# Performance work log

Hardware: AMD Instinct MI355X
Metric: run time of the kernel (lower is better)

Reference implementation:

```python
import jax, jax.numpy as jnp
import numpy as np

B, T = 8, 1024
BIG = 1e9

def _lin_init(k, fan_in, fan_out):
    return jax.random.normal(k, (fan_in, fan_out), dtype=jnp.float32) / np.sqrt(fan_in).astype(np.float32)

def setup_inputs() -> dict:
    key = jax.random.key(0)
    ks = jax.random.split(key, 10)
    return {
        "time_step": jax.random.uniform(ks[0], (B, T), dtype=jnp.float32),
        "event": jax.random.randint(ks[1], (B, T), 0, 4),
        "mkt_state": jax.random.randint(ks[2], (B, T), 0, 3),
        "mu_w1": _lin_init(ks[3], 4, 16), "mu_b1": jnp.zeros((16,), jnp.float32),
        "mu_w2": _lin_init(ks[4], 16, 1), "mu_b2": jnp.zeros((1,), jnp.float32),
        "a_w1": _lin_init(ks[5], 11, 16), "a_b1": jnp.zeros((16,), jnp.float32),
        "a_w2": _lin_init(ks[6], 16, 1), "a_b2": jnp.zeros((1,), jnp.float32),
        "d_w1": _lin_init(ks[7], 11, 16), "d_b1": jnp.zeros((16,), jnp.float32),
        "d_w2": _lin_init(ks[8], 16, 1), "d_b2": jnp.zeros((1,), jnp.float32),
    }

def _mlp(x, w1, b1, w2, b2):
    # Linear -> ReLU -> Linear -> Softplus
    return jax.nn.softplus(jax.nn.relu(x @ w1 + b1) @ w2 + b2)

def reference(time_step, event, mkt_state,
              mu_w1, mu_b1, mu_w2, mu_b2,
              a_w1, a_b1, a_w2, a_b2,
              d_w1, d_b1, d_w2, d_b2):
    Bs, Ts = event.shape
    I = Ts - 1  # number of source events
    seq_dt = time_step[:, 1:]                                   # [B, T-1]
    timestep = jnp.concatenate(
        [jnp.zeros((Bs, 1), seq_dt.dtype), jnp.cumsum(seq_dt, axis=-1)], axis=-1)  # [B, T]

    ev = jax.nn.one_hot(event, 4, dtype=jnp.float32)            # [B, T, 4]
    st = jax.nn.one_hot(mkt_state, 3, dtype=jnp.float32)        # [B, T, 3]
    eye4 = jnp.eye(4, dtype=jnp.float32)

    # relation_matrix[b,i,j] = [event_oh(b,i), state_oh(b,i), onehot(j)]  -> [B, I, 4, 11]
    rel = jnp.concatenate([
        jnp.broadcast_to(ev[:, :I, None, :], (Bs, I, 4, 4)),
        jnp.broadcast_to(st[:, :I, None, :], (Bs, I, 4, 3)),
        jnp.broadcast_to(eye4[None, None], (Bs, I, 4, 4)),
    ], axis=-1)

    # dt_matrix[b,i,t] = timestep[b,t] - timestep[b,i], non-positive -> BIG
    dt = timestep[:, None, :] - timestep[:, :I, None]           # [B, I, T]
    dt = jnp.where(dt > 0, dt, BIG)

    # mu: identical MLP applied to eye(4), broadcast to [B, T, 4, 1]
    mu_base = _mlp(eye4, mu_w1, mu_b1, mu_w2, mu_b2)            # [4, 1]
    mu = jnp.broadcast_to(mu_base[None, None], (Bs, Ts, 4, 1))

    alpha = jnp.swapaxes(_mlp(rel, a_w1, a_b1, a_w2, a_b2), 2, 3)  # [B, I, 1, 4]
    delta = jnp.swapaxes(_mlp(rel, d_w1, d_b1, d_w2, d_b2), 2, 3)  # [B, I, 1, 4]

    mask = jnp.triu(jnp.ones((I, I), jnp.float32))              # [I, J]
    dtj = dt[:, :, 1:, None]                                    # [B, I, J, 1]
    # causal exp-decay excitation summed over source events i
    excite = (alpha * jnp.exp(-delta * dtj) * mask[None, :, :, None]).sum(axis=1)  # [B, J, 4]

    intens_matrix = mu[:, 1:, :, 0] + excite                    # [B, T-1, 4]
    return (intens_matrix, mu, alpha, delta)
```

## Files before the change

### kernel.cpp

```cpp
#include <hip/hip_runtime.h>

#define TT 1024
#define BB 8
#define II 1023
#define OFF_INTENS 0
#define OFF_MU     32736
#define OFF_ALPHA  65504
#define OFF_DELTA  98240

__device__ __forceinline__ float softplus_f(float x) {
    return fmaxf(x, 0.f) + log1pf(expf(-fabsf(x)));
}

__global__ __launch_bounds__(256) void k_prep(
    const float* __restrict__ time_step,
    const float* __restrict__ mw1, const float* __restrict__ mb1,
    const float* __restrict__ mw2, const float* __restrict__ mb2,
    const float* __restrict__ aw1, const float* __restrict__ ab1,
    const float* __restrict__ aw2, const float* __restrict__ ab2,
    const float* __restrict__ dw1, const float* __restrict__ db1,
    const float* __restrict__ dw2, const float* __restrict__ db2,
    float* __restrict__ ws)
{
    __shared__ float lds[BB * TT];
    const int tid = threadIdx.x;
    for (int idx = tid; idx < BB * TT; idx += 256) lds[idx] = time_step[idx];
    __syncthreads();

    if (tid < 8) {
        const int b = tid;
        float run = 0.f;
        ws[b * TT] = 0.f;
        for (int t = 1; t < TT; ++t) {
            run += lds[b * TT + t];
            ws[b * TT + t] = run;
        }
    } else if (tid >= 64 && tid < 160) {
        const int idx = tid - 64;
        const int c   = (idx < 48) ? idx : idx - 48;
        const bool isA = idx < 48;
        const float* w1 = isA ? aw1 : dw1;
        const float* b1 = isA ? ab1 : db1;
        const float* w2 = isA ? aw2 : dw2;
        const float* b2 = isA ? ab2 : db2;
        const int e = c / 12, s = (c % 12) >> 2, k = c & 3;
        float acc = 0.f;
        #pragma unroll
        for (int n = 0; n < 16; ++n) {
            float h = w1[e * 16 + n] + w1[(4 + s) * 16 + n] + w1[(7 + k) * 16 + n] + b1[n];
            acc += fmaxf(h, 0.f) * w2[n];
        }
        ws[BB * TT + 2 * c + (isA ? 0 : 1)] = softplus_f(acc + b2[0]);
    } else if (tid >= 160 && tid < 164) {
        const int k = tid - 160;
        float acc = 0.f;
        #pragma unroll
        for (int n = 0; n < 16; ++n)
            acc += fmaxf(mw1[k * 16 + n] + mb1[n], 0.f) * mw2[n];
        ws[BB * TT + 96 + k] = softplus_f(acc + mb2[0]);
    }
}

__global__ __launch_bounds__(256) void k_main(
    const int* __restrict__ event, const int* __restrict__ mkt,
    const float* __restrict__ ws, float* __restrict__ out)
{
    __shared__ float  ts_l[TT];
    __shared__ float2 ad_l[TT * 4];
    const int tid = threadIdx.x;
    const int b   = blockIdx.y;
    const int jt  = blockIdx.x;
    const float2* adtab = (const float2*)(ws + BB * TT);
    const float*  mu_g  = ws + BB * TT + 96;

    for (int t = tid; t < TT; t += 256) ts_l[t] = ws[b * TT + t];
    for (int idx = tid; idx < TT * 4; idx += 256) {
        const int i = idx >> 2, k = idx & 3;
        const int e = event[b * TT + i];
        const int s = mkt[b * TT + i];
        ad_l[idx] = adtab[(e * 3 + s) * 4 + k];
    }
    __syncthreads();

    const int s  = tid & 3;
    const int k  = (tid >> 2) & 3;
    const int jj = tid >> 4;
    const int j  = jt * 16 + jj;

    float acc = 0.f;
    if (j < II) {
        const float tsj1 = ts_l[j + 1];
        #pragma unroll 4
        for (int i = s; i <= j; i += 4) {
            const float2 ad = ad_l[(i << 2) | k];
            float dt = tsj1 - ts_l[i];
            dt = (dt > 0.f) ? dt : 1e9f;
            acc += ad.x * __expf(-ad.y * dt);
        }
    }
    acc += __shfl_xor(acc, 1, 64);
    acc += __shfl_xor(acc, 2, 64);

    const float muk = mu_g[k];
    if (j < II) {
        const int base = (b * II + j) * 4 + k;
        if (s == 0)      out[OFF_INTENS + base] = muk + acc;
        else if (s == 1) out[OFF_ALPHA  + base] = ad_l[(j << 2) | k].x;
        else if (s == 2) out[OFF_DELTA  + base] = ad_l[(j << 2) | k].y;
    }
    if (s == 3) out[OFF_MU + (b * TT + j) * 4 + k] = muk;
}

extern "C" void kernel_launch(void* const* d_in, const int* in_sizes, int n_in,
                              void* d_out, int out_size, void* d_ws, size_t ws_size,
                              hipStream_t stream) {
    const float* time_step = (const float*)d_in[0];
    const int*   event     = (const int*)  d_in[1];
    const int*   mkt       = (const int*)  d_in[2];
    const float* mw1 = (const float*)d_in[3];
    const float* mb1 = (const float*)d_in[4];
    const float* mw2 = (const float*)d_in[5];
    const float* mb2 = (const float*)d_in[6];
    const float* aw1 = (const float*)d_in[7];
    const float* ab1 = (const float*)d_in[8];
    const float* aw2 = (const float*)d_in[9];
    const float* ab2 = (const float*)d_in[10];
    const float* dw1 = (const float*)d_in[11];
    const float* db1 = (const float*)d_in[12];
    const float* dw2 = (const float*)d_in[13];
    const float* db2 = (const float*)d_in[14];
    float* ws  = (float*)d_ws;
    float* out = (float*)d_out;

    k_prep<<<1, 256, 0, stream>>>(time_step, mw1, mb1, mw2, mb2,
                                  aw1, ab1, aw2, ab2, dw1, db1, dw2, db2, ws);
    k_main<<<dim3(64, 8), 256, 0, stream>>>(event, mkt, ws, out);
}
```

Before: 104.1 us.

## Fuse prep and main kernels, recompute prefix sums and MLP tables per block

Merges the single-block prep kernel into the main kernel. Each block now recomputes the tiny MLP lookup tables and the prefix sum of its batch row in shared memory, and the scan covers only the prefix that block needs. This removes one kernel launch, the serial one-block dependency and the round trip through global workspace. In exchange every block does redundant MLP work plus a serial scan by one thread of up to 1024 elements, which adds latency to the later j-tiles.

```diff
diff --git a/kernel.cpp b/kernel.cpp
--- a/kernel.cpp
+++ b/kernel.cpp
@@ -12,30 +12,30 @@
     return fmaxf(x, 0.f) + log1pf(expf(-fabsf(x)));
 }
 
-__global__ __launch_bounds__(256) void k_prep(
+__global__ __launch_bounds__(256) void k_fused(
     const float* __restrict__ time_step,
+    const int* __restrict__ event, const int* __restrict__ mkt,
     const float* __restrict__ mw1, const float* __restrict__ mb1,
     const float* __restrict__ mw2, const float* __restrict__ mb2,
     const float* __restrict__ aw1, const float* __restrict__ ab1,
     const float* __restrict__ aw2, const float* __restrict__ ab2,
     const float* __restrict__ dw1, const float* __restrict__ db1,
     const float* __restrict__ dw2, const float* __restrict__ db2,
-    float* __restrict__ ws)
+    float* __restrict__ out)
 {
-    __shared__ float lds[BB * TT];
+    __shared__ float  raw[TT];
+    __shared__ float  pre[TT];
+    __shared__ float2 tab[48];
+    __shared__ float  mu_s[4];
+    __shared__ float2 ad_l[TT * 4];
+
     const int tid = threadIdx.x;
-    for (int idx = tid; idx < BB * TT; idx += 256) lds[idx] = time_step[idx];
-    __syncthreads();
+    const int jt  = blockIdx.x;
+    const int b   = blockIdx.y;
 
-    if (tid < 8) {
-        const int b = tid;
-        float run = 0.f;
-        ws[b * TT] = 0.f;
-        for (int t = 1; t < TT; ++t) {
-            run += lds[b * TT + t];
-            ws[b * TT + t] = run;
-        }
-    } else if (tid >= 64 && tid < 160) {
+    ((float4*)raw)[tid] = ((const float4*)(time_step + b * TT))[tid];
+
+    if (tid >= 64 && tid < 160) {
         const int idx = tid - 64;
         const int c   = (idx < 48) ? idx : idx - 48;
         const bool isA = idx < 48;
@@ -50,35 +50,48 @@
             float h = w1[e * 16 + n] + w1[(4 + s) * 16 + n] + w1[(7 + k) * 16 + n] + b1[n];
             acc += fmaxf(h, 0.f) * w2[n];
         }
-        ws[BB * TT + 2 * c + (isA ? 0 : 1)] = softplus_f(acc + b2[0]);
+        const float v = softplus_f(acc + b2[0]);
+        if (isA) tab[c].x = v; else tab[c].y = v;
     } else if (tid >= 160 && tid < 164) {
         const int k = tid - 160;
         float acc = 0.f;
         #pragma unroll
         for (int n = 0; n < 16; ++n)
             acc += fmaxf(mw1[k * 16 + n] + mb1[n], 0.f) * mw2[n];
-        ws[BB * TT + 96 + k] = softplus_f(acc + mb2[0]);
+        mu_s[k] = softplus_f(acc + mb2[0]);
     }
-}
+    __syncthreads();
 
-__global__ __launch_bounds__(256) void k_main(
-    const int* __restrict__ event, const int* __restrict__ mkt,
-    const float* __restrict__ ws, float* __restrict__ out)
-{
-    __shared__ float  ts_l[TT];
-    __shared__ float2 ad_l[TT * 4];
-    const int tid = threadIdx.x;
-    const int b   = blockIdx.y;
-    const int jt  = blockIdx.x;
-    const float2* adtab = (const float2*)(ws + BB * TT);
-    const float*  mu_g  = ws + BB * TT + 96;
-
-    for (int t = tid; t < TT; t += 256) ts_l[t] = ws[b * TT + t];
-    for (int idx = tid; idx < TT * 4; idx += 256) {
-        const int i = idx >> 2, k = idx & 3;
-        const int e = event[b * TT + i];
-        const int s = mkt[b * TT + i];
-        ad_l[idx] = adtab[(e * 3 + s) * 4 + k];
+    if (tid == 0) {
+        const int need = min(jt * 16 + 17, TT);
+        const float4* r4 = (const float4*)raw;
+        float4*       p4 = (float4*)pre;
+        float run = 0.f;
+        for (int t0 = 0; t0 < need; t0 += 16) {
+            const int q = t0 >> 2;
+            const float4 va = r4[q], vb = r4[q + 1], vc = r4[q + 2], vd = r4[q + 3];
+            const float v[16] = {va.x, va.y, va.z, va.w, vb.x, vb.y, vb.z, vb.w,
+                                 vc.x, vc.y, vc.z, vc.w, vd.x, vd.y, vd.z, vd.w};
+            float o[16];
+            #pragma unroll
+            for (int u = 0; u < 16; ++u) {
+                run += (t0 + u == 0) ? 0.f : v[u];
+                o[u] = run;
+            }
+            p4[q]     = make_float4(o[0],  o[1],  o[2],  o[3]);
+            p4[q + 1] = make_float4(o[4],  o[5],  o[6],  o[7]);
+            p4[q + 2] = make_float4(o[8],  o[9],  o[10], o[11]);
+            p4[q + 3] = make_float4(o[12], o[13], o[14], o[15]);
+        }
+    } else if (tid >= 64) {
+        const int t = tid - 64;
+        for (int i = t; i < TT; i += 192) {
+            const int c = (event[b * TT + i] * 3 + mkt[b * TT + i]) << 2;
+            const float2 v0 = tab[c], v1 = tab[c + 1], v2 = tab[c + 2], v3 = tab[c + 3];
+            float4* dst = (float4*)&ad_l[i << 2];
+            dst[0] = make_float4(v0.x, v0.y, v1.x, v1.y);
+            dst[1] = make_float4(v2.x, v2.y, v3.x, v3.y);
+        }
     }
     __syncthreads();
 
@@ -89,11 +102,11 @@
 
     float acc = 0.f;
     if (j < II) {
-        const float tsj1 = ts_l[j + 1];
+        const float tsj1 = pre[j + 1];
         #pragma unroll 4
         for (int i = s; i <= j; i += 4) {
             const float2 ad = ad_l[(i << 2) | k];
-            float dt = tsj1 - ts_l[i];
+            float dt = tsj1 - pre[i];
             dt = (dt > 0.f) ? dt : 1e9f;
             acc += ad.x * __expf(-ad.y * dt);
         }
@@ -101,7 +114,7 @@
     acc += __shfl_xor(acc, 1, 64);
     acc += __shfl_xor(acc, 2, 64);
 
-    const float muk = mu_g[k];
+    const float muk = mu_s[k];
     if (j < II) {
         const int base = (b * II + j) * 4 + k;
         if (s == 0)      out[OFF_INTENS + base] = muk + acc;
@@ -129,10 +142,10 @@
     const float* db1 = (const float*)d_in[12];
     const float* dw2 = (const float*)d_in[13];
     const float* db2 = (const float*)d_in[14];
-    float* ws  = (float*)d_ws;
     float* out = (float*)d_out;
 
-    k_prep<<<1, 256, 0, stream>>>(time_step, mw1, mb1, mw2, mb2,
-                                  aw1, ab1, aw2, ab2, dw1, db1, dw2, db2, ws);
-    k_main<<<dim3(64, 8), 256, 0, stream>>>(event, mkt, ws, out);
+    k_fused<<<dim3(64, 8), 256, 0, stream>>>(time_step, event, mkt,
+                                             mw1, mb1, mw2, mb2,
+                                             aw1, ab1, aw2, ab2,
+                                             dw1, db1, dw2, db2, out);
 }
```

New measurement: 100.5 us. 3.4% less time.
